# Kernel optimization log

Measured on AMD Instinct MI355X. Metric: run time of the kernel, lower is better.

## Reference

```python
import jax, jax.numpy as jnp
import numpy as np

B, L, H = 8, 2048, 1024
MASK_IDENTITY = True


def setup_inputs() -> dict:
    key = jax.random.key(0)
    ks = jax.random.split(key, 7)
    s = 1.0 / np.sqrt(H)
    return {
        "x": jax.random.normal(ks[0], (B, L, H), dtype=jnp.float32),
        "Wq": jax.random.uniform(ks[1], (H, H), jnp.float32, -s, s),
        "bq": jax.random.uniform(ks[2], (H,), jnp.float32, -s, s),
        "Wk": jax.random.uniform(ks[3], (H, H), jnp.float32, -s, s),
        "bk": jax.random.uniform(ks[4], (H,), jnp.float32, -s, s),
        "Wv": jax.random.uniform(ks[5], (H, H), jnp.float32, -s, s),
        "bv": jax.random.uniform(ks[6], (H,), jnp.float32, -s, s),
    }


def reference(x, Wq, bq, Wk, bk, Wv, bv):
    # Linear layers (torch Linear: y = x @ W.T + b)
    q = jnp.einsum("blh,oh->blo", x, Wq) + bq
    k = jnp.einsum("blh,oh->blo", x, Wk) + bk
    v = jnp.einsum("blh,oh->blo", x, Wv) + bv
    hidden = q.shape[-1]
    # NOTE: original scales by hidden_size, not sqrt(hidden_size)
    attn = jnp.einsum("blh,bmh->blm", q / hidden, k)  # [B, L, L]
    if MASK_IDENTITY:
        mask_value = -jnp.finfo(attn.dtype).max
        eye = jnp.eye(attn.shape[-1], dtype=bool)  # [L, L]
        attn = jnp.where(eye[None, :, :], mask_value, attn)
    attn = jax.nn.softmax(attn, axis=-1)
    return jnp.einsum("blm,bmh->blh", attn, v)
```

## Files before the change

### kernel.cpp

```cpp
#include <hip/hip_runtime.h>


typedef unsigned short u16;
typedef __bf16 bfx8 __attribute__((ext_vector_type(8)));
typedef float f32x4 __attribute__((ext_vector_type(4)));

__device__ __forceinline__ u16 f2bf(float f) {
    unsigned int x = __float_as_uint(f);
    unsigned int r = (x + 0x7fffu + ((x >> 16) & 1u)) >> 16;
    return (u16)r;
}
__device__ __forceinline__ float bf2f(u16 u) {
    return __uint_as_float(((unsigned int)u) << 16);
}

__global__ void f32_to_bf16(const float* __restrict__ src, u16* __restrict__ dst, int n8) {
    int i = blockIdx.x * blockDim.x + threadIdx.x;
    if (i < n8) {
        float4 a = ((const float4*)src)[i * 2];
        float4 b = ((const float4*)src)[i * 2 + 1];
        ushort4 lo; lo.x = f2bf(a.x); lo.y = f2bf(a.y); lo.z = f2bf(a.z); lo.w = f2bf(a.w);
        ushort4 hi; hi.x = f2bf(b.x); hi.y = f2bf(b.y); hi.z = f2bf(b.z); hi.w = f2bf(b.w);
        ((ushort4*)dst)[i * 2] = lo;
        ((ushort4*)dst)[i * 2 + 1] = hi;
    }
}

__global__ void transpose_bf16(const u16* __restrict__ src, u16* __restrict__ dst) {
    __shared__ u16 s[64][64 + 8];
    int z = blockIdx.z;
    int tm = blockIdx.x * 64;
    int th = blockIdx.y * 64;
    const u16* sp = src + (long)z * 2048 * 1024;
    u16* dp = dst + (long)z * 1024 * 2048;
    int t = threadIdx.x;
#pragma unroll
    for (int p = 0; p < 4; ++p) {
        int r = p * 16 + (t >> 4);
        int c = (t & 15) * 4;
        ushort4 v = *(const ushort4*)(sp + (long)(tm + r) * 1024 + th + c);
        s[r][c] = v.x; s[r][c + 1] = v.y; s[r][c + 2] = v.z; s[r][c + 3] = v.w;
    }
    __syncthreads();
#pragma unroll
    for (int p = 0; p < 4; ++p) {
        int hr = p * 16 + (t >> 4);
        int c = (t & 15) * 4;
        ushort4 v;
        v.x = s[c][hr]; v.y = s[c + 1][hr]; v.z = s[c + 2][hr]; v.w = s[c + 3][hr];
        *(ushort4*)(dp + (long)(th + hr) * 2048 + tm + c) = v;
    }
}


#define PH_MID() do{ asm volatile("" ::: "memory"); __builtin_amdgcn_s_barrier(); \
    asm volatile("s_waitcnt lgkmcnt(0)" ::: "memory"); __builtin_amdgcn_sched_barrier(0); \
    __builtin_amdgcn_s_setprio(1); }while(0)
#define PH_END() do{ __builtin_amdgcn_s_setprio(0); asm volatile("" ::: "memory"); \
    __builtin_amdgcn_s_barrier(); }while(0)

#define RD_A(cur, mibase) do{ \
    const char* _b = smem + (cur)*65536 + (wr*128 + (mibase)*16 + rA)*128; \
    a[0][0] = *(const bfx8*)(_b + 0*2048 + ofk0); a[0][1] = *(const bfx8*)(_b + 0*2048 + ofk1); \
    a[1][0] = *(const bfx8*)(_b + 1*2048 + ofk0); a[1][1] = *(const bfx8*)(_b + 1*2048 + ofk1); \
    a[2][0] = *(const bfx8*)(_b + 2*2048 + ofk0); a[2][1] = *(const bfx8*)(_b + 2*2048 + ofk1); \
    a[3][0] = *(const bfx8*)(_b + 3*2048 + ofk0); a[3][1] = *(const bfx8*)(_b + 3*2048 + ofk1); \
}while(0)

#define RD_B(cur, nibase) do{ \
    const char* _b = smem + (cur)*65536 + 32768 + (wc*64 + (nibase)*16 + rA)*128; \
    b[(nibase)+0][0] = *(const bfx8*)(_b + 0*2048 + ofk0); b[(nibase)+0][1] = *(const bfx8*)(_b + 0*2048 + ofk1); \
    b[(nibase)+1][0] = *(const bfx8*)(_b + 1*2048 + ofk0); b[(nibase)+1][1] = *(const bfx8*)(_b + 1*2048 + ofk1); \
}while(0)

#define MMQ(M0, N0) do{ \
    _Pragma("unroll") \
    for (int ks = 0; ks < 2; ++ks) \
    _Pragma("unroll") \
    for (int mi = 0; mi < 4; ++mi) \
    _Pragma("unroll") \
    for (int ni = 0; ni < 2; ++ni) \
        acc[(M0)+mi][(N0)+ni] = __builtin_amdgcn_mfma_f32_16x16x32_bf16(a[mi][ks], b[(N0)+ni][ks], acc[(M0)+mi][(N0)+ni], 0, 0, 0); \
}while(0)

template <int MODE>
__global__ __launch_bounds__(512, 2) void gemm8(
    const u16* __restrict__ Ab, const u16* __restrict__ Bb,
    int K, int lda, int ldb,
    long strideA, long strideB,
    const float* __restrict__ biasCat,
    u16* __restrict__ outBf, long strideP,
    float* __restrict__ den,
    float* __restrict__ outF)
{
    __shared__ __align__(16) char smem[131072];
    const int tid  = threadIdx.x;
    const int lane = tid & 63;
    const int wid  = tid >> 6;
    const int wr = wid >> 2, wc = wid & 3;
    const int z = blockIdx.z;
    const u16* A = Ab + (long)z * strideA + (long)blockIdx.x * 256 * lda;
    const u16* B = Bb + (long)z * strideB + (long)blockIdx.y * 256 * ldb;
    const int NT = K >> 6;

    const int rA  = lane & 15;
    const int cg  = lane >> 4;
    const int swz = rA & 7;
    const int ofk0 = ((cg)     ^ swz) << 4;
    const int ofk1 = ((cg | 4) ^ swz) << 4;

    f32x4 acc[8][4] = {};
    bfx8 a[4][2], b[4][2];

    auto stage = [&](int buf, int isB, int half, int t) {
        const u16* src = isB ? B : A;
        const int ld = isB ? ldb : lda;
#pragma unroll
        for (int rnd = 0; rnd < 2; ++rnd) {
            int c = rnd * 512 + tid;
            int row = half * 128 + (c >> 3);
            int slot = c & 7;
            const u16* g = src + (long)row * ld + t * 64 + ((slot ^ (row & 7)) << 3);
            char* l = (char*)smem + buf * 65536 + isB * 32768 + half * 16384 + rnd * 8192 + wid * 1024;
            __builtin_amdgcn_global_load_lds((__attribute__((address_space(1))) void*)g,
                                             (__attribute__((address_space(3))) void*)l, 16, 0, 0);
        }
    };

    stage(0, 0, 0, 0); stage(0, 0, 1, 0); stage(0, 1, 0, 0); stage(0, 1, 1, 0);
    stage(1, 1, 0, 1); stage(1, 1, 1, 1);
    asm volatile("s_waitcnt vmcnt(4)" ::: "memory");
    __builtin_amdgcn_s_barrier();

    int cur = 0;
    for (int t = 0; t < NT; ++t) {
        const int nxt = cur ^ 1;
        RD_A(cur, 0); RD_B(cur, 0);
        if (t + 1 < NT) stage(nxt, 0, 0, t + 1);
        PH_MID(); MMQ(0, 0); PH_END();
        RD_B(cur, 2);
        if (t + 1 < NT) stage(nxt, 0, 1, t + 1);
        PH_MID(); MMQ(0, 2); PH_END();
        RD_A(cur, 4);
        if (t + 2 < NT) stage(cur, 1, 0, t + 2);
        PH_MID(); MMQ(4, 2); PH_END();
        if (t + 2 < NT) stage(cur, 1, 1, t + 2);
        asm volatile("s_waitcnt vmcnt(4)" ::: "memory");
        PH_MID(); MMQ(4, 0); PH_END();
        cur = nxt;
    }

    const int r0 = blockIdx.x * 256 + wr * 128 + (cg << 2);
    const int c0 = blockIdx.y * 256 + wc * 64 + rA;
#pragma unroll
    for (int mi = 0; mi < 8; ++mi) {
#pragma unroll
        for (int r = 0; r < 4; ++r) {
            const int grow = r0 + mi * 16 + r;
            if constexpr (MODE == 0) {
#pragma unroll
                for (int ni = 0; ni < 4; ++ni) {
                    int gcol = c0 + ni * 16;
                    float v = acc[mi][ni][r] + biasCat[gcol];
                    if (gcol < 1024) v *= (1.0f / 1024.0f);
                    int which = gcol >> 10;
                    long dst = (long)which * (16384L * 1024) + (long)grow * 1024 + (gcol & 1023);
                    outBf[dst] = f2bf(v);
                }
            } else if constexpr (MODE == 1) {
                float s = 0.0f;
#pragma unroll
                for (int ni = 0; ni < 4; ++ni) {
                    int gcol = c0 + ni * 16;
                    float p = (grow == gcol) ? 0.0f : __expf(acc[mi][ni][r]);
                    u16 pb = f2bf(p);
                    outBf[(long)z * strideP + (long)grow * 2048 + gcol] = pb;
                    s += bf2f(pb);
                }
                s += __shfl_xor(s, 1); s += __shfl_xor(s, 2);
                s += __shfl_xor(s, 4); s += __shfl_xor(s, 8);
                if (rA == 0) atomicAdd(&den[z * 2048 + grow], s);
            } else {
                float d = den[z * 2048 + grow];
#pragma unroll
                for (int ni = 0; ni < 4; ++ni)
                    outF[(long)z * (2048L * 1024) + (long)grow * 1024 + (c0 + ni * 16)] = acc[mi][ni][r] / d;
            }
        }
    }
}

extern "C" void kernel_launch(void* const* d_in, const int* in_sizes, int n_in,
                              void* d_out, int out_size, void* d_ws, size_t ws_size,
                              hipStream_t stream) {
    const float* x  = (const float*)d_in[0];
    const float* Wq = (const float*)d_in[1];
    const float* bq = (const float*)d_in[2];
    const float* Wk = (const float*)d_in[3];
    const float* bk = (const float*)d_in[4];
    const float* Wv = (const float*)d_in[5];
    const float* bv = (const float*)d_in[6];
    float* out = (float*)d_out;

    const long XB_OFF   = 0;
    const long WB_OFF   = 33554432;
    const long BIAS_OFF = WB_OFF + 6291456;
    const long DEN_OFF  = BIAS_OFF + 12288;
    const long QKV_OFF  = DEN_OFF + 65536;
    const long PB_OFF   = QKV_OFF + 2L * 33554432;
    const unsigned long long NEED = (unsigned long long)(PB_OFF + 67108864);
    if (ws_size < NEED) return;

    char* ws = (char*)d_ws;
    u16*   xb      = (u16*)(ws + XB_OFF);
    u16*   vT      = (u16*)(ws + XB_OFF);
    u16*   Wb      = (u16*)(ws + WB_OFF);
    float* biasCat = (float*)(ws + BIAS_OFF);
    float* den     = (float*)(ws + DEN_OFF);
    u16*   qkv     = (u16*)(ws + QKV_OFF);
    u16*   qb = qkv;
    u16*   kb = qkv + 16384L * 1024;
    u16*   vb = qkv + 2L * 16384 * 1024;
    u16*   Pb = (u16*)(ws + PB_OFF);

    f32_to_bf16<<<8192, 256, 0, stream>>>(x, xb, 2097152);
    f32_to_bf16<<<512, 256, 0, stream>>>(Wq, Wb, 131072);
    f32_to_bf16<<<512, 256, 0, stream>>>(Wk, Wb + 1048576, 131072);
    f32_to_bf16<<<512, 256, 0, stream>>>(Wv, Wb + 2097152, 131072);
    hipMemcpyAsync(biasCat,        bq, 4096, hipMemcpyDeviceToDevice, stream);
    hipMemcpyAsync(biasCat + 1024, bk, 4096, hipMemcpyDeviceToDevice, stream);
    hipMemcpyAsync(biasCat + 2048, bv, 4096, hipMemcpyDeviceToDevice, stream);
    hipMemsetAsync(den, 0, 65536, stream);

    gemm8<0><<<dim3(64, 12, 1), 512, 0, stream>>>(
        xb, Wb, 1024, 1024, 1024, 0, 0, biasCat, qkv, 0, nullptr, nullptr);

    transpose_bf16<<<dim3(32, 16, 8), 256, 0, stream>>>(vb, vT);

    gemm8<1><<<dim3(8, 8, 8), 512, 0, stream>>>(
        qb, kb, 1024, 1024, 1024, 2048L * 1024, 2048L * 1024,
        nullptr, Pb, 2048L * 2048, den, nullptr);

    gemm8<2><<<dim3(8, 4, 8), 512, 0, stream>>>(
        Pb, vT, 2048, 2048, 2048, 2048L * 2048, 1024L * 2048,
        nullptr, nullptr, 0, den, out);
}
```

Measured before the change: 389.2 us.

## Restructure GEMM main loop into ping-pong tiles with register double-buffered A fragments

Replaces the single shared-memory array and lambda staging with four separate LDS buffers and a manually unrolled two-tile loop. A fragments are double-buffered in registers (aA/aB), so the next tile's A rows are read while the current tile's MFMAs run. Whole A/B tiles are restaged as a unit after a full vmcnt(0) wait, rather than in half-tile pieces. The aim is better overlap of LDS reads and global-to-LDS loads with MFMA work. The cost is more registers and a stricter wait point that could stall on outstanding loads.

```diff
diff --git a/kernel.cpp b/kernel.cpp
--- a/kernel.cpp
+++ b/kernel.cpp
@@ -53,38 +53,67 @@
 }
 
 
-#define PH_MID() do{ asm volatile("" ::: "memory"); __builtin_amdgcn_s_barrier(); \
-    asm volatile("s_waitcnt lgkmcnt(0)" ::: "memory"); __builtin_amdgcn_sched_barrier(0); \
-    __builtin_amdgcn_s_setprio(1); }while(0)
-#define PH_END() do{ __builtin_amdgcn_s_setprio(0); asm volatile("" ::: "memory"); \
-    __builtin_amdgcn_s_barrier(); }while(0)
-
-#define RD_A(cur, mibase) do{ \
-    const char* _b = smem + (cur)*65536 + (wr*128 + (mibase)*16 + rA)*128; \
-    a[0][0] = *(const bfx8*)(_b + 0*2048 + ofk0); a[0][1] = *(const bfx8*)(_b + 0*2048 + ofk1); \
-    a[1][0] = *(const bfx8*)(_b + 1*2048 + ofk0); a[1][1] = *(const bfx8*)(_b + 1*2048 + ofk1); \
-    a[2][0] = *(const bfx8*)(_b + 2*2048 + ofk0); a[2][1] = *(const bfx8*)(_b + 2*2048 + ofk1); \
-    a[3][0] = *(const bfx8*)(_b + 3*2048 + ofk0); a[3][1] = *(const bfx8*)(_b + 3*2048 + ofk1); \
-}while(0)
-
-#define RD_B(cur, nibase) do{ \
-    const char* _b = smem + (cur)*65536 + 32768 + (wc*64 + (nibase)*16 + rA)*128; \
-    b[(nibase)+0][0] = *(const bfx8*)(_b + 0*2048 + ofk0); b[(nibase)+0][1] = *(const bfx8*)(_b + 0*2048 + ofk1); \
-    b[(nibase)+1][0] = *(const bfx8*)(_b + 1*2048 + ofk0); b[(nibase)+1][1] = *(const bfx8*)(_b + 1*2048 + ofk1); \
-}while(0)
-
-#define MMQ(M0, N0) do{ \
+#define FENCE asm volatile("" ::: "memory")
+#define BAR   __builtin_amdgcn_s_barrier()
+#define PRIO1 __builtin_amdgcn_s_setprio(1)
+#define PRIO0 __builtin_amdgcn_s_setprio(0)
+
+#define STAGEF(DST, SRC, LD, tt) do{ \
+    _Pragma("unroll") \
+    for (int rnd = 0; rnd < 4; ++rnd) { \
+        int c_ = rnd * 512 + tid; \
+        int row_ = c_ >> 3; \
+        int slot_ = c_ & 7; \
+        const u16* g_ = (SRC) + (long)row_ * (LD) + (tt) * 64 + ((slot_ ^ (row_ & 7)) << 3); \
+        char* l_ = (char*)(DST) + rnd * 8192 + wid * 1024; \
+        __builtin_amdgcn_global_load_lds((__attribute__((address_space(1))) void*)g_, \
+            (__attribute__((address_space(3))) void*)l_, 16, 0, 0); \
+    } \
+}while(0)
+
+#define RD_A4(dst, SARR, mibase) do{ \
+    const char* _b = (const char*)(SARR) + ((wr * 128 + (mibase) * 16 + rA) * 128); \
+    dst[0][0] = *(const bfx8*)(_b + 0 * 2048 + ofk0); dst[0][1] = *(const bfx8*)(_b + 0 * 2048 + ofk1); \
+    dst[1][0] = *(const bfx8*)(_b + 1 * 2048 + ofk0); dst[1][1] = *(const bfx8*)(_b + 1 * 2048 + ofk1); \
+    dst[2][0] = *(const bfx8*)(_b + 2 * 2048 + ofk0); dst[2][1] = *(const bfx8*)(_b + 2 * 2048 + ofk1); \
+    dst[3][0] = *(const bfx8*)(_b + 3 * 2048 + ofk0); dst[3][1] = *(const bfx8*)(_b + 3 * 2048 + ofk1); \
+}while(0)
+
+#define RD_B2(dst, SARR, nibase) do{ \
+    const char* _b = (const char*)(SARR) + ((wc * 64 + (nibase) * 16 + rA) * 128); \
+    dst[0][0] = *(const bfx8*)(_b + 0 * 2048 + ofk0); dst[0][1] = *(const bfx8*)(_b + 0 * 2048 + ofk1); \
+    dst[1][0] = *(const bfx8*)(_b + 1 * 2048 + ofk0); dst[1][1] = *(const bfx8*)(_b + 1 * 2048 + ofk1); \
+}while(0)
+
+#define MMQ(AS, BS, M0, N0) do{ \
     _Pragma("unroll") \
     for (int ks = 0; ks < 2; ++ks) \
     _Pragma("unroll") \
     for (int mi = 0; mi < 4; ++mi) \
     _Pragma("unroll") \
     for (int ni = 0; ni < 2; ++ni) \
-        acc[(M0)+mi][(N0)+ni] = __builtin_amdgcn_mfma_f32_16x16x32_bf16(a[mi][ks], b[(N0)+ni][ks], acc[(M0)+mi][(N0)+ni], 0, 0, 0); \
+        acc[(M0)+mi][(N0)+ni] = __builtin_amdgcn_mfma_f32_16x16x32_bf16(AS[mi][ks], BS[ni][ks], acc[(M0)+mi][(N0)+ni], 0, 0, 0); \
+}while(0)
+
+#define TILE(SA_R, SB_R, SA_O, tt) do{ \
+     \
+    RD_B2(b01, SB_R, 0); RD_B2(b23, SB_R, 2); \
+    FENCE; BAR; PRIO1; MMQ(aA, b01, 0, 0); PRIO0; FENCE; BAR; \
+     \
+    RD_A4(aB, SA_R, 4); \
+    FENCE; BAR; PRIO1; MMQ(aA, b23, 0, 2); PRIO0; FENCE; BAR; \
+     \
+    asm volatile("s_waitcnt vmcnt(0)" ::: "memory"); \
+    if ((tt) + 2 < NT) STAGEF(SB_R, B, ldb, (tt) + 2); \
+    FENCE; BAR; PRIO1; MMQ(aB, b23, 4, 2); PRIO0; FENCE; BAR; \
+     \
+    RD_A4(aA, SA_O, 0); \
+    if ((tt) + 2 < NT) STAGEF(SA_R, A, lda, (tt) + 2); \
+    FENCE; BAR; PRIO1; MMQ(aB, b01, 4, 0); PRIO0; FENCE; BAR; \
 }while(0)
 
 template <int MODE>
-__global__ __launch_bounds__(512, 2) void gemm8(
+__global__ __launch_bounds__(512, 2) void gemm8p(
     const u16* __restrict__ Ab, const u16* __restrict__ Bb,
     int K, int lda, int ldb,
     long strideA, long strideB,
@@ -93,7 +122,11 @@
     float* __restrict__ den,
     float* __restrict__ outF)
 {
-    __shared__ __align__(16) char smem[131072];
+    __shared__ __align__(16) u16 sA0[16384];
+    __shared__ __align__(16) u16 sB0[16384];
+    __shared__ __align__(16) u16 sA1[16384];
+    __shared__ __align__(16) u16 sB1[16384];
+
     const int tid  = threadIdx.x;
     const int lane = tid & 63;
     const int wid  = tid >> 6;
@@ -110,44 +143,18 @@
     const int ofk1 = ((cg | 4) ^ swz) << 4;
 
     f32x4 acc[8][4] = {};
-    bfx8 a[4][2], b[4][2];
-
-    auto stage = [&](int buf, int isB, int half, int t) {
-        const u16* src = isB ? B : A;
-        const int ld = isB ? ldb : lda;
-#pragma unroll
-        for (int rnd = 0; rnd < 2; ++rnd) {
-            int c = rnd * 512 + tid;
-            int row = half * 128 + (c >> 3);
-            int slot = c & 7;
-            const u16* g = src + (long)row * ld + t * 64 + ((slot ^ (row & 7)) << 3);
-            char* l = (char*)smem + buf * 65536 + isB * 32768 + half * 16384 + rnd * 8192 + wid * 1024;
-            __builtin_amdgcn_global_load_lds((__attribute__((address_space(1))) void*)g,
-                                             (__attribute__((address_space(3))) void*)l, 16, 0, 0);
-        }
-    };
-
-    stage(0, 0, 0, 0); stage(0, 0, 1, 0); stage(0, 1, 0, 0); stage(0, 1, 1, 0);
-    stage(1, 1, 0, 1); stage(1, 1, 1, 1);
-    asm volatile("s_waitcnt vmcnt(4)" ::: "memory");
-    __builtin_amdgcn_s_barrier();
-
-    int cur = 0;
-    for (int t = 0; t < NT; ++t) {
-        const int nxt = cur ^ 1;
-        RD_A(cur, 0); RD_B(cur, 0);
-        if (t + 1 < NT) stage(nxt, 0, 0, t + 1);
-        PH_MID(); MMQ(0, 0); PH_END();
-        RD_B(cur, 2);
-        if (t + 1 < NT) stage(nxt, 0, 1, t + 1);
-        PH_MID(); MMQ(0, 2); PH_END();
-        RD_A(cur, 4);
-        if (t + 2 < NT) stage(cur, 1, 0, t + 2);
-        PH_MID(); MMQ(4, 2); PH_END();
-        if (t + 2 < NT) stage(cur, 1, 1, t + 2);
-        asm volatile("s_waitcnt vmcnt(4)" ::: "memory");
-        PH_MID(); MMQ(4, 0); PH_END();
-        cur = nxt;
+    bfx8 aA[4][2], aB[4][2], b01[2][2], b23[2][2];
+
+    STAGEF(sA0, A, lda, 0); STAGEF(sB0, B, ldb, 0);
+    STAGEF(sA1, A, lda, 1); STAGEF(sB1, B, ldb, 1);
+    asm volatile("s_waitcnt vmcnt(8)" ::: "memory");
+    BAR;
+    RD_A4(aA, sA0, 0);
+    FENCE;
+
+    for (int t = 0; t < NT; t += 2) {
+        TILE(sA0, sB0, sA1, t);
+        TILE(sA1, sB1, sA0, t + 1);
     }
 
     const int r0 = blockIdx.x * 256 + wr * 128 + (cg << 2);
@@ -232,16 +239,16 @@
     hipMemcpyAsync(biasCat + 2048, bv, 4096, hipMemcpyDeviceToDevice, stream);
     hipMemsetAsync(den, 0, 65536, stream);
 
-    gemm8<0><<<dim3(64, 12, 1), 512, 0, stream>>>(
+    gemm8p<0><<<dim3(64, 12, 1), 512, 0, stream>>>(
         xb, Wb, 1024, 1024, 1024, 0, 0, biasCat, qkv, 0, nullptr, nullptr);
 
     transpose_bf16<<<dim3(32, 16, 8), 256, 0, stream>>>(vb, vT);
 
-    gemm8<1><<<dim3(8, 8, 8), 512, 0, stream>>>(
+    gemm8p<1><<<dim3(8, 8, 8), 512, 0, stream>>>(
         qb, kb, 1024, 1024, 1024, 2048L * 1024, 2048L * 1024,
         nullptr, Pb, 2048L * 2048, den, nullptr);
 
-    gemm8<2><<<dim3(8, 4, 8), 512, 0, stream>>>(
+    gemm8p<2><<<dim3(8, 4, 8), 512, 0, stream>>>(
         Pb, vT, 2048, 2048, 2048, 2048L * 2048, 1024L * 2048,
         nullptr, nullptr, 0, den, out);
 }
```

New measurement: 406.7 us. 1.04x slower.
